# Kernel optimization log

Measured on AMD Instinct MI355X. Metric: run time of the kernel, lower is better.

The kernel has to match this reference:

```python
import jax, jax.numpy as jnp
import numpy as np

N_NODES = 100000
NNZ = 1600000
IN_CH = 256
OUT_CH = 64  # heads * out_channels, heads=1


def setup_inputs() -> dict:
    key = jax.random.key(0)
    k1, k2, k3, k4, k5 = jax.random.split(key, 5)
    X = jax.random.normal(k1, (N_NODES, IN_CH), dtype=jnp.float32)
    # nn.Linear(in, heads*out, bias=False) weight: [out, in]
    W_lin = jax.random.normal(k2, (OUT_CH, IN_CH), dtype=jnp.float32) * (1.0 / np.sqrt(IN_CH))
    # sparse Laplacian L in COO form
    L_rows = jax.random.randint(k3, (NNZ,), 0, N_NODES, dtype=jnp.int64)
    L_cols = jax.random.randint(k4, (NNZ,), 0, N_NODES, dtype=jnp.int64)
    L_vals = jax.random.uniform(k5, (NNZ,), dtype=jnp.float32)
    return {"g1": 0, "g2": 0, "X": X, "W_lin": W_lin,
            "L_rows": L_rows, "L_cols": L_cols, "L_vals": L_vals}


def reference(g1, g2, X, W_lin, L_rows, L_cols, L_vals):
    # dense projection: X @ W^T  -> [N, out]
    Xp = jnp.einsum('ni,oi->no', X, W_lin)
    # SpMM: Xv = L @ Xp, COO gather-scale-scatter
    gathered = L_vals[:, None] * Xp[L_cols]            # [nnz, out]
    Xv = jax.ops.segment_sum(gathered, L_rows, num_segments=N_NODES)
    return Xv
```

## Files before the change

kernel.cpp:

```cpp
#include <hip/hip_runtime.h>

#define N_IN_CH 256
#define N_OUT_CH 64
#define BROW 128
#define NBK 1024
#define B1_T 256
#define B1_PT 16
#define B1_E 4096
#define ECAP 4096
#define OVFCAP 65536
#define NGEMM 512

typedef __attribute__((ext_vector_type(8))) short short8;
typedef __attribute__((ext_vector_type(4))) float f32x4;

__device__ inline ushort f2bf(float f) {
    unsigned u = __float_as_uint(f);
    return (ushort)((u + 0x7FFFu + ((u >> 16) & 1u)) >> 16);
}
__device__ inline float bf2f(ushort u) {
    return __uint_as_float(((unsigned)u) << 16);
}

__global__ __launch_bounds__(256, 4) void fused_kernel(const float* __restrict__ X,
        const float* __restrict__ W, ushort* __restrict__ Xp, int nrows, int ngemm,
        const int* __restrict__ rows, const int* __restrict__ cols,
        const float* __restrict__ vals, int* __restrict__ bcur,
        int* __restrict__ ovfcnt, int4* __restrict__ ovf,
        int2* __restrict__ colbuf, int nnz, int nb) {
    __shared__ union SM {
        ushort ws[64 * 256];
        struct { int cnt[NBK]; int base[NBK]; } b;
    } sm;
    const int tid = threadIdx.x;

    if (blockIdx.x < ngemm) {
        #pragma unroll
        for (int it = 0; it < 16; ++it) {
            int f = it * 256 + tid;
            int n = f >> 6, c4 = f & 63;
            float4 w = *(const float4*)&W[n * N_IN_CH + c4 * 4];
            ushort4 u;
            u.x = f2bf(w.x); u.y = f2bf(w.y); u.z = f2bf(w.z); u.w = f2bf(w.w);
            int byteoff = (n << 9) | (((c4 << 3)) ^ ((n & 7) << 4));
            *(ushort4*)((char*)sm.ws + byteoff) = u;
        }
        __syncthreads();

        const int wave = tid >> 6, lane = tid & 63;
        const int ml = lane & 15, q = lane >> 4;
        const int swz = (ml & 7) << 4;
        const int q16 = q << 4;
        const int ntiles = (nrows + 15) >> 4;
        const int nw = ngemm * 4;
        int t = blockIdx.x * 4 + wave;

        const char* wsb = (const char*)sm.ws;
        float4 raw[16];

        if (t < ntiles) {
            int gr0 = t * 16 + ml;
            if (gr0 < nrows) {
                const float* xr = X + (size_t)gr0 * N_IN_CH + q * 8;
                #pragma unroll
                for (int kt = 0; kt < 8; ++kt) {
                    raw[2 * kt]     = *(const float4*)&xr[kt * 32];
                    raw[2 * kt + 1] = *(const float4*)&xr[kt * 32 + 4];
                }
            } else {
                #pragma unroll
                for (int i = 0; i < 16; ++i) raw[i] = make_float4(0.f, 0.f, 0.f, 0.f);
            }
        }

        while (t < ntiles) {
            const int tn = t + nw;
            const int grn = tn * 16 + ml;
            const bool okn = grn < nrows;
            const float* xrn = X + (size_t)grn * N_IN_CH + q * 8;

            f32x4 acc[4];
            #pragma unroll
            for (int nt = 0; nt < 4; ++nt) acc[nt] = (f32x4){0.f, 0.f, 0.f, 0.f};

            #pragma unroll
            for (int kt = 0; kt < 8; ++kt) {
                float4 f0 = raw[2 * kt], f1 = raw[2 * kt + 1];
                short8 s;
                s[0] = (short)f2bf(f0.x); s[1] = (short)f2bf(f0.y);
                s[2] = (short)f2bf(f0.z); s[3] = (short)f2bf(f0.w);
                s[4] = (short)f2bf(f1.x); s[5] = (short)f2bf(f1.y);
                s[6] = (short)f2bf(f1.z); s[7] = (short)f2bf(f1.w);
                if (tn < ntiles) {
                    if (okn) {
                        raw[2 * kt]     = *(const float4*)&xrn[kt * 32];
                        raw[2 * kt + 1] = *(const float4*)&xrn[kt * 32 + 4];
                    } else {
                        raw[2 * kt]     = make_float4(0.f, 0.f, 0.f, 0.f);
                        raw[2 * kt + 1] = make_float4(0.f, 0.f, 0.f, 0.f);
                    }
                }
                #pragma unroll
                for (int nt = 0; nt < 4; ++nt) {
                    short8 b = *(const short8*)(wsb + ((nt * 16 + ml) << 9)
                                                + (((kt << 6) | q16) ^ swz));
                    acc[nt] = __builtin_amdgcn_mfma_f32_16x16x32_bf16(s, b, acc[nt], 0, 0, 0);
                }
            }

            #pragma unroll
            for (int nt = 0; nt < 4; ++nt) {
                #pragma unroll
                for (int reg = 0; reg < 4; ++reg) {
                    int gr = t * 16 + q * 4 + reg;
                    if (gr < nrows)
                        Xp[(size_t)gr * N_OUT_CH + nt * 16 + ml] = f2bf(acc[nt][reg]);
                }
            }
            t = tn;
        }
    } else {
        for (int i = tid; i < nb; i += B1_T) sm.b.cnt[i] = 0;
        __syncthreads();

        const int e = (blockIdx.x - ngemm) * B1_E + tid * B1_PT;
        int nval = nnz - e;
        if (nval > B1_PT) nval = B1_PT;
        if (nval < 0) nval = 0;

        int r[B1_PT], c[B1_PT]; float v[B1_PT];
        if (nval == B1_PT) {
            #pragma unroll
            for (int j = 0; j < B1_PT / 4; ++j) {
                *(int4*)&r[4 * j] = *(const int4*)&rows[e + 4 * j];
                *(int4*)&c[4 * j] = *(const int4*)&cols[e + 4 * j];
                *(float4*)&v[4 * j] = *(const float4*)&vals[e + 4 * j];
            }
        } else {
            #pragma unroll
            for (int j = 0; j < B1_PT; ++j)
                if (j < nval) { r[j] = rows[e + j]; c[j] = cols[e + j]; v[j] = vals[e + j]; }
        }

        #pragma unroll
        for (int j = 0; j < B1_PT; ++j)
            if (j < nval) atomicAdd(&sm.b.cnt[r[j] >> 7], 1);
        __syncthreads();

        for (int i = tid; i < nb; i += B1_T) {
            int cn = sm.b.cnt[i];
            sm.b.base[i] = cn ? atomicAdd(&bcur[i], cn) : 0;
            sm.b.cnt[i] = 0;
        }
        __syncthreads();

        #pragma unroll
        for (int j = 0; j < B1_PT; ++j) {
            if (j < nval) {
                int b = r[j] >> 7;
                int pib = sm.b.base[b] + atomicAdd(&sm.b.cnt[b], 1);
                if (pib < ECAP) {
                    int2 cv;
                    cv.x = c[j] | ((r[j] & 127) << 17);
                    cv.y = __float_as_int(v[j]);
                    colbuf[(size_t)b * ECAP + pib] = cv;
                } else {
                    int op = atomicAdd(ovfcnt, 1);
                    if (op < OVFCAP) {
                        int4 o; o.x = r[j]; o.y = c[j];
                        o.z = __float_as_int(v[j]); o.w = 0;
                        ovf[op] = o;
                    }
                }
            }
        }
    }
}

__global__ __launch_bounds__(512) void bspmm_kernel(const int* __restrict__ bcur,
        const int2* __restrict__ colbuf, const ushort* __restrict__ Xp,
        float* __restrict__ out, int nrows, const int* __restrict__ ovfcnt,
        const int4* __restrict__ ovf) {
    __shared__ int2 ebuf[ECAP];
    __shared__ int rc[BROW];
    __shared__ int rb[BROW + 1];
    const int b = blockIdx.x, t = threadIdx.x;
    const int ne = min(bcur[b], ECAP);
    const int2* cb = colbuf + (size_t)b * ECAP;
    const int row0 = b * BROW;

    int2 ev[8];
    const int ebase = t * 8;
    int ecnt = ne - ebase;
    if (ecnt > 8) ecnt = 8;
    if (ecnt < 0) ecnt = 0;
    if (ecnt == 8) {
        #pragma unroll
        for (int j = 0; j < 4; ++j)
            *(int4*)&ev[2 * j] = *(const int4*)&cb[ebase + 2 * j];
    } else {
        #pragma unroll
        for (int j = 0; j < 8; ++j)
            if (j < ecnt) ev[j] = cb[ebase + j];
    }

    if (t < BROW) rc[t] = 0;
    __syncthreads();
    #pragma unroll
    for (int j = 0; j < 8; ++j)
        if (j < ecnt) atomicAdd(&rc[(ev[j].x >> 17) & (BROW - 1)], 1);
    __syncthreads();
    int c0 = (t < BROW) ? rc[t] : 0;
    #pragma unroll
    for (int d = 1; d < BROW; d <<= 1) {
        int a = (t < BROW && t >= d) ? rc[t - d] : 0;
        __syncthreads();
        if (t < BROW) rc[t] += a;
        __syncthreads();
    }
    if (t < BROW) rb[t] = rc[t] - c0;
    if (t == 0) rb[BROW] = ne;
    __syncthreads();
    if (t < BROW) rc[t] = 0;
    __syncthreads();
    #pragma unroll
    for (int j = 0; j < 8; ++j) {
        if (j < ecnt) {
            int rl = (ev[j].x >> 17) & (BROW - 1);
            int pos = rb[rl] + atomicAdd(&rc[rl], 1);
            ebuf[pos] = ev[j];
        }
    }
    __syncthreads();

    const int wave = t >> 6;
    const int q4 = (t >> 4) & 3;
    const int l16 = t & 15;
    const int qr0 = wave * 16 + q4 * 4;
    int i = rb[qr0];
    const int e = rb[qr0 + 4];
    float4 acc = make_float4(0.f, 0.f, 0.f, 0.f);
    int cur = -1;

    for (; i + 8 <= e; i += 8) {
        int2 cv[8];
        #pragma unroll
        for (int j = 0; j < 8; ++j) cv[j] = ebuf[i + j];
        ushort4 xv[8];
        #pragma unroll
        for (int j = 0; j < 8; ++j)
            xv[j] = *(const ushort4*)&Xp[(size_t)(cv[j].x & 0x1FFFF) * N_OUT_CH + l16 * 4];
        #pragma unroll
        for (int j = 0; j < 8; ++j) {
            int rl = (cv[j].x >> 17) & (BROW - 1);
            if (rl != cur) {
                if (cur >= 0)
                    *(float4*)&out[(size_t)(row0 + cur) * N_OUT_CH + l16 * 4] = acc;
                cur = rl;
                acc = make_float4(0.f, 0.f, 0.f, 0.f);
            }
            float vv = __int_as_float(cv[j].y);
            acc.x += vv * bf2f(xv[j].x);
            acc.y += vv * bf2f(xv[j].y);
            acc.z += vv * bf2f(xv[j].z);
            acc.w += vv * bf2f(xv[j].w);
        }
    }
    for (; i < e; ++i) {
        int2 cv = ebuf[i];
        int rl = (cv.x >> 17) & (BROW - 1);
        if (rl != cur) {
            if (cur >= 0)
                *(float4*)&out[(size_t)(row0 + cur) * N_OUT_CH + l16 * 4] = acc;
            cur = rl;
            acc = make_float4(0.f, 0.f, 0.f, 0.f);
        }
        ushort4 xv = *(const ushort4*)&Xp[(size_t)(cv.x & 0x1FFFF) * N_OUT_CH + l16 * 4];
        float vv = __int_as_float(cv.y);
        acc.x += vv * bf2f(xv.x);
        acc.y += vv * bf2f(xv.y);
        acc.z += vv * bf2f(xv.z);
        acc.w += vv * bf2f(xv.w);
    }
    if (cur >= 0)
        *(float4*)&out[(size_t)(row0 + cur) * N_OUT_CH + l16 * 4] = acc;

    #pragma unroll
    for (int r = 0; r < 4; ++r) {
        int lr = qr0 + r;
        if (rb[lr] == rb[lr + 1]) {
            int gr = row0 + lr;
            if (gr < nrows)
                *(float4*)&out[(size_t)gr * N_OUT_CH + l16 * 4] =
                    make_float4(0.f, 0.f, 0.f, 0.f);
        }
    }

    __syncthreads();
    const int lane = t & 63;
    int n = min(ovfcnt[0], OVFCAP);
    for (int e2 = wave; e2 < n; e2 += 8) {
        int4 v = ovf[e2];
        if ((v.x >> 7) == b)
            atomicAdd(&out[(size_t)v.x * N_OUT_CH + lane],
                      __int_as_float(v.z) * bf2f(Xp[(size_t)v.y * N_OUT_CH + lane]));
    }
}

__global__ __launch_bounds__(256) void spmm_atomic_kernel(const int* __restrict__ rows,
        const int* __restrict__ cols, const float* __restrict__ vals,
        const ushort* __restrict__ Xp, float* __restrict__ out, int nnz) {
    int t = blockIdx.x * blockDim.x + threadIdx.x;
    int e = t >> 6;
    int c = t & 63;
    if (e < nnz) {
        atomicAdd(&out[(size_t)rows[e] * N_OUT_CH + c],
                  vals[e] * bf2f(Xp[(size_t)cols[e] * N_OUT_CH + c]));
    }
}

extern "C" void kernel_launch(void* const* d_in, const int* in_sizes, int n_in,
                              void* d_out, int out_size, void* d_ws, size_t ws_size,
                              hipStream_t stream) {
    const float* X      = (const float*)d_in[2];
    const float* W      = (const float*)d_in[3];
    const int*   L_rows = (const int*)d_in[4];
    const int*   L_cols = (const int*)d_in[5];
    const float* L_vals = (const float*)d_in[6];
    float* out = (float*)d_out;

    const int nrows = in_sizes[2] / N_IN_CH;
    const int nnz   = in_sizes[4];
    const int nb    = (nrows + BROW - 1) / BROW;

    size_t off_xp  = 0;
    size_t xp_b    = (size_t)nrows * N_OUT_CH * 2;
    size_t off_bc  = off_xp + ((xp_b + 15) & ~(size_t)15);
    size_t off_ov  = off_bc + (((size_t)(nb + 1) * 4 + 15) & ~(size_t)15);
    size_t off_cv  = off_ov + (size_t)OVFCAP * 16;
    size_t need    = off_cv + (size_t)nb * ECAP * 8;

    ushort* Xp = (ushort*)((char*)d_ws + off_xp);
    const bool binned = (ws_size >= need && nb <= NBK);
    int* bcur = (int*)((char*)d_ws + off_bc);

    int ntiles = (nrows + 15) >> 4;
    int ngemm = NGEMM;
    int maxg = (ntiles + 3) / 4;
    if (ngemm > maxg) ngemm = maxg;

    if (binned) {
        int*  ovfcnt = bcur + nb;
        int4* ovf    = (int4*)((char*)d_ws + off_ov);
        int2* colbuf = (int2*)((char*)d_ws + off_cv);
        int nbin = (nnz + B1_E - 1) / B1_E;

        hipMemsetAsync(bcur, 0, (size_t)(nb + 1) * 4, stream);
        fused_kernel<<<ngemm + nbin, 256, 0, stream>>>(X, W, Xp, nrows, ngemm,
                L_rows, L_cols, L_vals, bcur, ovfcnt, ovf, colbuf, nnz, nb);
        bspmm_kernel<<<nb, 512, 0, stream>>>(bcur, colbuf, Xp, out, nrows, ovfcnt, ovf);
    } else {
        fused_kernel<<<ngemm, 256, 0, stream>>>(X, W, Xp, nrows, ngemm,
                nullptr, nullptr, nullptr, nullptr, nullptr, nullptr, nullptr, 0, 0);
        hipMemsetAsync(d_out, 0, (size_t)out_size * sizeof(float), stream);
        long long total = (long long)nnz * 64;
        spmm_atomic_kernel<<<(int)((total + 255) / 256), 256, 0, stream>>>(
            L_rows, L_cols, L_vals, Xp, out, nnz);
    }
}
```

Baseline: 287.4 us.

## Stream X tiles into LDS with async global_load_lds double buffering

The GEMM phase now loads X rows straight into per-wave LDS staging buffers with global_load_lds, splitting each 16-row tile into four K-chunks that are double-buffered. The next chunk, or the first chunk of the next tile, is issued before compute and gated by explicit vmcnt waits. This replaces the 16 float4 register prefetch that inflated VGPR use. The number of GEMM blocks is halved, and the occupancy hint is dropped from launch_bounds because LDS use grows by 32KB per block. The risk is lower occupancy, extra LDS traffic, and the reliance on a hand-written waitcnt that must be correct for loads issued per lane.

```diff
diff --git a/kernel.cpp b/kernel.cpp
--- a/kernel.cpp
+++ b/kernel.cpp
@@ -9,10 +9,17 @@
 #define B1_E 4096
 #define ECAP 4096
 #define OVFCAP 65536
-#define NGEMM 512
+#define NGEMM 256
 
 typedef __attribute__((ext_vector_type(8))) short short8;
 typedef __attribute__((ext_vector_type(4))) float f32x4;
+
+typedef const __attribute__((address_space(1))) void gas_void;
+typedef __attribute__((address_space(3))) void las_void;
+
+__device__ inline void gload16(const void* g, void* l) {
+    __builtin_amdgcn_global_load_lds((gas_void*)g, (las_void*)l, 16, 0, 0);
+}
 
 __device__ inline ushort f2bf(float f) {
     unsigned u = __float_as_uint(f);
@@ -22,16 +29,15 @@
     return __uint_as_float(((unsigned)u) << 16);
 }
 
-__global__ __launch_bounds__(256, 4) void fused_kernel(const float* __restrict__ X,
+__global__ __launch_bounds__(256) void fused_kernel(const float* __restrict__ X,
         const float* __restrict__ W, ushort* __restrict__ Xp, int nrows, int ngemm,
         const int* __restrict__ rows, const int* __restrict__ cols,
         const float* __restrict__ vals, int* __restrict__ bcur,
         int* __restrict__ ovfcnt, int4* __restrict__ ovf,
         int2* __restrict__ colbuf, int nnz, int nb) {
-    __shared__ union SM {
-        ushort ws[64 * 256];
-        struct { int cnt[NBK]; int base[NBK]; } b;
-    } sm;
+    struct GemmSM { ushort ws[64 * 256]; char stage[4][2][4096]; };
+    struct BinSM  { int cnt[NBK]; int base[NBK]; };
+    __shared__ union { GemmSM g; BinSM b; } sm;
     const int tid = threadIdx.x;
 
     if (blockIdx.x < ngemm) {
@@ -42,69 +48,67 @@
             float4 w = *(const float4*)&W[n * N_IN_CH + c4 * 4];
             ushort4 u;
             u.x = f2bf(w.x); u.y = f2bf(w.y); u.z = f2bf(w.z); u.w = f2bf(w.w);
-            int byteoff = (n << 9) | (((c4 << 3)) ^ ((n & 7) << 4));
-            *(ushort4*)((char*)sm.ws + byteoff) = u;
+            int boff = (n << 9) | ((c4 << 3) ^ ((n & 7) << 4));
+            *(ushort4*)((char*)sm.g.ws + boff) = u;
         }
         __syncthreads();
 
         const int wave = tid >> 6, lane = tid & 63;
         const int ml = lane & 15, q = lane >> 4;
         const int swz = (ml & 7) << 4;
-        const int q16 = q << 4;
         const int ntiles = (nrows + 15) >> 4;
-        const int nw = ngemm * 4;
+        const int nwv = ngemm * 4;
+        const char* wsp = (const char*)sm.g.ws;
         int t = blockIdx.x * 4 + wave;
 
-        const char* wsb = (const char*)sm.ws;
-        float4 raw[16];
-
-        if (t < ntiles) {
-            int gr0 = t * 16 + ml;
-            if (gr0 < nrows) {
-                const float* xr = X + (size_t)gr0 * N_IN_CH + q * 8;
+#define ISSUE_CHUNK(tt, cc, bb)                                              \
+        do {                                                                 \
+            int rowl_ = (tt) * 16 + ml;                                      \
+            if (rowl_ >= nrows) rowl_ = nrows - 1;                           \
+            const float* gb_ = X + (size_t)rowl_ * N_IN_CH + (cc) * 64 + q * 8; \
+            char* lb_ = sm.g.stage[wave][bb];                                \
+            gload16(gb_,      lb_);                                          \
+            gload16(gb_ + 4,  lb_ + 1024);                                   \
+            gload16(gb_ + 32, lb_ + 2048);                                   \
+            gload16(gb_ + 36, lb_ + 3072);                                   \
+        } while (0)
+
+        if (t < ntiles) ISSUE_CHUNK(t, 0, 0);
+
+        while (t < ntiles) {
+            f32x4 acc[4];
+            #pragma unroll
+            for (int nt = 0; nt < 4; ++nt) acc[nt] = (f32x4){0.f, 0.f, 0.f, 0.f};
+
+            #pragma unroll
+            for (int c = 0; c < 4; ++c) {
+                const int cur = c & 1;
+                bool hn;
+                if (c < 3) { ISSUE_CHUNK(t, c + 1, cur ^ 1); hn = true; }
+                else if (t + nwv < ntiles) { ISSUE_CHUNK(t + nwv, 0, cur ^ 1); hn = true; }
+                else hn = false;
+                if (hn) asm volatile("s_waitcnt vmcnt(4)" ::: "memory");
+                else    asm volatile("s_waitcnt vmcnt(0)" ::: "memory");
+                __builtin_amdgcn_sched_barrier(0);
+
                 #pragma unroll
-                for (int kt = 0; kt < 8; ++kt) {
-                    raw[2 * kt]     = *(const float4*)&xr[kt * 32];
-                    raw[2 * kt + 1] = *(const float4*)&xr[kt * 32 + 4];
-                }
-            } else {
-                #pragma unroll
-                for (int i = 0; i < 16; ++i) raw[i] = make_float4(0.f, 0.f, 0.f, 0.f);
-            }
-        }
-
-        while (t < ntiles) {
-            const int tn = t + nw;
-            const int grn = tn * 16 + ml;
-            const bool okn = grn < nrows;
-            const float* xrn = X + (size_t)grn * N_IN_CH + q * 8;
-
-            f32x4 acc[4];
-            #pragma unroll
-            for (int nt = 0; nt < 4; ++nt) acc[nt] = (f32x4){0.f, 0.f, 0.f, 0.f};
-
-            #pragma unroll
-            for (int kt = 0; kt < 8; ++kt) {
-                float4 f0 = raw[2 * kt], f1 = raw[2 * kt + 1];
-                short8 s;
-                s[0] = (short)f2bf(f0.x); s[1] = (short)f2bf(f0.y);
-                s[2] = (short)f2bf(f0.z); s[3] = (short)f2bf(f0.w);
-                s[4] = (short)f2bf(f1.x); s[5] = (short)f2bf(f1.y);
-                s[6] = (short)f2bf(f1.z); s[7] = (short)f2bf(f1.w);
-                if (tn < ntiles) {
-                    if (okn) {
-                        raw[2 * kt]     = *(const float4*)&xrn[kt * 32];
-                        raw[2 * kt + 1] = *(const float4*)&xrn[kt * 32 + 4];
-                    } else {
-                        raw[2 * kt]     = make_float4(0.f, 0.f, 0.f, 0.f);
-                        raw[2 * kt + 1] = make_float4(0.f, 0.f, 0.f, 0.f);
+                for (int ktl = 0; ktl < 2; ++ktl) {
+                    const char* sb = sm.g.stage[wave][cur] + ktl * 2048 + lane * 16;
+                    float4 lo = *(const float4*)sb;
+                    float4 hi = *(const float4*)(sb + 1024);
+                    short8 s;
+                    s[0] = (short)f2bf(lo.x); s[1] = (short)f2bf(lo.y);
+                    s[2] = (short)f2bf(lo.z); s[3] = (short)f2bf(lo.w);
+                    s[4] = (short)f2bf(hi.x); s[5] = (short)f2bf(hi.y);
+                    s[6] = (short)f2bf(hi.z); s[7] = (short)f2bf(hi.w);
+                    const int kt = 2 * c + ktl;
+                    const int x0 = (kt << 6) | (q << 4);
+                    #pragma unroll
+                    for (int nt = 0; nt < 4; ++nt) {
+                        short8 b = *(const short8*)(wsp + ((nt * 16 + ml) << 9)
+                                                    + (x0 ^ swz));
+                        acc[nt] = __builtin_amdgcn_mfma_f32_16x16x32_bf16(s, b, acc[nt], 0, 0, 0);
                     }
-                }
-                #pragma unroll
-                for (int nt = 0; nt < 4; ++nt) {
-                    short8 b = *(const short8*)(wsb + ((nt * 16 + ml) << 9)
-                                                + (((kt << 6) | q16) ^ swz));
-                    acc[nt] = __builtin_amdgcn_mfma_f32_16x16x32_bf16(s, b, acc[nt], 0, 0, 0);
                 }
             }
 
@@ -117,8 +121,9 @@
                         Xp[(size_t)gr * N_OUT_CH + nt * 16 + ml] = f2bf(acc[nt][reg]);
                 }
             }
-            t = tn;
-        }
+            t += nwv;
+        }
+#undef ISSUE_CHUNK
     } else {
         for (int i = tid; i < nb; i += B1_T) sm.b.cnt[i] = 0;
         __syncthreads();
```

Result: faster. 245.8 us (-14.5%).
